# Kernel tuning notes

Hardware: AMD Instinct MI355X
Metric: run time of the kernel (lower is better)

## Reference

```python
import jax, jax.numpy as jnp
import numpy as np

T, M = 64, 64
ROI, SPA, WORD, I3D = 2048, 4, 300, 1024
H, D = 512, 256  # so_hidden, so_out_dim (= rel_dim)
IN = ROI + SPA + WORD  # 2352


def _w(k, shape):
    return jax.random.normal(k, shape, dtype=jnp.float32) * 0.02


def setup_inputs() -> dict:
    key = jax.random.key(0)
    ks = jax.random.split(key, 32)
    inp = {
        "roi_feats": jax.random.normal(ks[0], (T, M, ROI), dtype=jnp.float32),
        "spatial": jax.random.uniform(ks[1], (T, M, SPA), dtype=jnp.float32),
        "i3d_feats": jax.random.normal(ks[2], (T, I3D), dtype=jnp.float32),
        "subj_emb": jax.random.normal(ks[3], (WORD,), dtype=jnp.float32),
        "obj_emb": jax.random.normal(ks[4], (WORD,), dtype=jnp.float32),
        "pred_emb": jax.random.normal(ks[5], (WORD,), dtype=jnp.float32),
        # subject / object encoders (torch Linear convention: W is (out,in))
        "subj_w1": _w(ks[6], (H, IN)), "subj_b1": _w(ks[7], (H,)),
        "subj_w2": _w(ks[8], (D, H)), "subj_b2": _w(ks[9], (D,)),
        "obj_w1": _w(ks[10], (H, IN)), "obj_b1": _w(ks[11], (H,)),
        "obj_w2": _w(ks[12], (D, H)), "obj_b2": _w(ks[13], (D,)),
        # fuse MLPs (in = 2*D)
        "fuse_s_w1": _w(ks[14], (H, 2 * D)), "fuse_s_b1": _w(ks[15], (H,)),
        "fuse_s_w2": _w(ks[16], (D, H)), "fuse_s_b2": _w(ks[17], (D,)),
        "fuse_o_w1": _w(ks[18], (H, 2 * D)), "fuse_o_b1": _w(ks[19], (H,)),
        "fuse_o_w2": _w(ks[20], (D, H)), "fuse_o_b2": _w(ks[21], (D,)),
        # relation projections + MLP
        "W_rs": _w(ks[22], (D, D)),
        "W_ro": _w(ks[23], (D, D)),
        "rel_w1": _w(ks[24], (H, D + WORD)), "rel_b1": _w(ks[25], (H,)),
        "rel_w2": _w(ks[26], (D, H)), "rel_b2": _w(ks[27], (D,)),
    }
    return inp


def _linear(x, W, b):
    return x @ W.T + b


def _mlp2(x, w1, b1, w2, b2):
    return _linear(jax.nn.relu(_linear(x, w1, b1)), w2, b2)


def reference(roi_feats, spatial, i3d_feats, subj_emb, obj_emb, pred_emb,
              subj_w1, subj_b1, subj_w2, subj_b2,
              obj_w1, obj_b1, obj_w2, obj_b2,
              fuse_s_w1, fuse_s_b1, fuse_s_w2, fuse_s_b2,
              fuse_o_w1, fuse_o_b1, fuse_o_w2, fuse_o_b2,
              W_rs, W_ro, rel_w1, rel_b1, rel_w2, rel_b2):
    Tn, Mn, _ = roi_feats.shape
    se = jnp.broadcast_to(subj_emb, (Tn, Mn, subj_emb.shape[-1]))
    oe = jnp.broadcast_to(obj_emb, (Tn, Mn, obj_emb.shape[-1]))
    # SubjectObjectEncoder: fc2(relu(fc1([roi; spa; word])))
    fs_base = _mlp2(jnp.concatenate([roi_feats, spatial, se], axis=-1),
                    subj_w1, subj_b1, subj_w2, subj_b2)  # (T,M,D)
    fo_base = _mlp2(jnp.concatenate([roi_feats, spatial, oe], axis=-1),
                    obj_w1, obj_b1, obj_w2, obj_b2)
    # use_gsa = use_lla = False -> fuse([base; base])
    fs = _mlp2(jnp.concatenate([fs_base, fs_base], axis=-1),
               fuse_s_w1, fuse_s_b1, fuse_s_w2, fuse_s_b2)
    fo = _mlp2(jnp.concatenate([fo_base, fo_base], axis=-1),
               fuse_o_w1, fuse_o_b1, fuse_o_w2, fuse_o_b2)
    # Eq. 15: pairwise diff + predicate word, then 2-layer MLP
    fs_proj = fs @ W_rs.T
    fo_proj = fo @ W_ro.T
    diff = fs_proj[:, :, None, :] - fo_proj[:, None, :, :]  # (T,M,M,D)
    # rel_fc1([diff; pred]) split into diff part + constant pred part
    Wd, Wp = rel_w1[:, :fs.shape[-1]], rel_w1[:, fs.shape[-1]:]
    h = jax.nn.relu(diff @ Wd.T + (pred_emb @ Wp.T + rel_b1))  # (T,M,M,H)
    return h @ rel_w2.T + rel_b2  # (T,M,M,D)
```

## Files before the change

kernel.cpp:

```cpp
#include <hip/hip_runtime.h>
#include <hip/hip_bf16.h>

typedef __attribute__((ext_vector_type(4))) float f32x4;
typedef __attribute__((ext_vector_type(8))) short s16x8;

__device__ __forceinline__ void async_lds16(const void* g, void* l) {
  __builtin_amdgcn_global_load_lds((const __attribute__((address_space(1))) void*)g,
                                   (__attribute__((address_space(3))) void*)l, 16, 0, 0);
}

__device__ __forceinline__ short f2bf(float x) {
  __hip_bfloat16 h = __float2bfloat16(x);
  short s;
  __builtin_memcpy(&s, &h, 2);
  return s;
}

__device__ __forceinline__ s16x8 pack8(f32x4 a, f32x4 b) {
  s16x8 r;
  r[0] = f2bf(a[0]); r[1] = f2bf(a[1]); r[2] = f2bf(a[2]); r[3] = f2bf(a[3]);
  r[4] = f2bf(b[0]); r[5] = f2bf(b[1]); r[6] = f2bf(b[2]); r[7] = f2bf(b[3]);
  return r;
}

template<bool RELU, bool OUT_BF16, bool HAS_BIAS>
__global__ __launch_bounds__(256) void gemm_bt(
    const __hip_bfloat16* __restrict__ Ag, const __hip_bfloat16* __restrict__ Bg,
    const float* __restrict__ biasg, void* __restrict__ Cg,
    int lda, int ldb, int K, int ldc,
    int strideA, int strideB, int strideBias, long strideC)
{
  __shared__ __align__(16) short As[4096];
  __shared__ __align__(16) short Bs[4096];
  const int tid  = threadIdx.x;
  const int lane = tid & 63;
  const int wid  = tid >> 6;
  const int z    = blockIdx.z;
  const __hip_bfloat16* A = Ag + (long)z * strideA;
  const __hip_bfloat16* B = Bg + (long)z * strideB;
  const float* bias = HAS_BIAS ? (biasg + (long)z * strideBias) : nullptr;
  const int row0 = blockIdx.y * 128;
  const int col0 = blockIdx.x * 128;

  const int srow = wid * 16 + (lane >> 2);
  const int scol = (lane & 3) * 8;

  f32x4 acc[4][4];
#pragma unroll
  for (int i = 0; i < 4; ++i)
#pragma unroll
    for (int j = 0; j < 4; ++j) acc[i][j] = (f32x4)(0.0f);

  const int rw = (wid & 1) * 64;
  const int cw = (wid >> 1) * 64;
  const int lm = lane & 15;
  const int kg = (lane >> 4) * 8;

  for (int ks = 0; ks < K; ks += 32) {
    __syncthreads();
#pragma unroll
    for (int is = 0; is < 2; ++is) {
      async_lds16(A + (long)(row0 + is * 64 + srow) * lda + ks + scol,
                  (char*)As + is * 4096 + wid * 1024);
      async_lds16(B + (long)(col0 + is * 64 + srow) * ldb + ks + scol,
                  (char*)Bs + is * 4096 + wid * 1024);
    }
    __syncthreads();
    s16x8 af[4], bf[4];
#pragma unroll
    for (int mt = 0; mt < 4; ++mt)
      af[mt] = *(const s16x8*)(As + (rw + mt * 16 + lm) * 32 + kg);
#pragma unroll
    for (int nt = 0; nt < 4; ++nt)
      bf[nt] = *(const s16x8*)(Bs + (cw + nt * 16 + lm) * 32 + kg);
#pragma unroll
    for (int mt = 0; mt < 4; ++mt)
#pragma unroll
      for (int nt = 0; nt < 4; ++nt)
        acc[mt][nt] = __builtin_amdgcn_mfma_f32_16x16x32_bf16(af[mt], bf[nt], acc[mt][nt], 0, 0, 0);
  }

  const int lr4 = (lane >> 4) * 4;
#pragma unroll
  for (int mt = 0; mt < 4; ++mt) {
#pragma unroll
    for (int nt = 0; nt < 4; ++nt) {
      const int col = col0 + cw + nt * 16 + lm;
      const float bv = HAS_BIAS ? bias[col] : 0.0f;
#pragma unroll
      for (int r = 0; r < 4; ++r) {
        const int row = row0 + rw + mt * 16 + lr4 + r;
        float v = acc[mt][nt][r] + bv;
        if (RELU) v = fmaxf(v, 0.0f);
        if (OUT_BF16)
          ((__hip_bfloat16*)Cg)[(long)z * strideC + (long)row * ldc + col] = __float2bfloat16(v);
        else
          ((float*)Cg)[(long)z * strideC + (long)row * ldc + col] = v;
      }
    }
  }
}

template<bool RELU, bool OUT_BF16, bool HAS_BIAS>
__global__ __launch_bounds__(256) void gemm_bt64(
    const __hip_bfloat16* __restrict__ Ag, const __hip_bfloat16* __restrict__ Bg,
    const float* __restrict__ biasg, void* __restrict__ Cg,
    int lda, int ldb, int K, int ldc,
    int strideA, int strideB, int strideBias, long strideC)
{
  __shared__ __align__(16) short As[2048];
  __shared__ __align__(16) short Bs[2048];
  const int tid  = threadIdx.x;
  const int lane = tid & 63;
  const int wid  = tid >> 6;
  const int z    = blockIdx.z;
  const __hip_bfloat16* A = Ag + (long)z * strideA;
  const __hip_bfloat16* B = Bg + (long)z * strideB;
  const float* bias = HAS_BIAS ? (biasg + (long)z * strideBias) : nullptr;
  const int row0 = blockIdx.y * 64;
  const int col0 = blockIdx.x * 64;

  const int srow = wid * 16 + (lane >> 2);
  const int scol = (lane & 3) * 8;

  f32x4 acc[2][2];
#pragma unroll
  for (int i = 0; i < 2; ++i)
#pragma unroll
    for (int j = 0; j < 2; ++j) acc[i][j] = (f32x4)(0.0f);

  const int rw = (wid & 1) * 32;
  const int cw = (wid >> 1) * 32;
  const int lm = lane & 15;
  const int kg = (lane >> 4) * 8;

  for (int ks = 0; ks < K; ks += 32) {
    __syncthreads();
    async_lds16(A + (long)(row0 + srow) * lda + ks + scol, (char*)As + wid * 1024);
    async_lds16(B + (long)(col0 + srow) * ldb + ks + scol, (char*)Bs + wid * 1024);
    __syncthreads();
    s16x8 af[2], bf[2];
#pragma unroll
    for (int mt = 0; mt < 2; ++mt)
      af[mt] = *(const s16x8*)(As + (rw + mt * 16 + lm) * 32 + kg);
#pragma unroll
    for (int nt = 0; nt < 2; ++nt)
      bf[nt] = *(const s16x8*)(Bs + (cw + nt * 16 + lm) * 32 + kg);
#pragma unroll
    for (int mt = 0; mt < 2; ++mt)
#pragma unroll
      for (int nt = 0; nt < 2; ++nt)
        acc[mt][nt] = __builtin_amdgcn_mfma_f32_16x16x32_bf16(af[mt], bf[nt], acc[mt][nt], 0, 0, 0);
  }

  const int lr4 = (lane >> 4) * 4;
#pragma unroll
  for (int mt = 0; mt < 2; ++mt) {
#pragma unroll
    for (int nt = 0; nt < 2; ++nt) {
      const int col = col0 + cw + nt * 16 + lm;
      const float bv = HAS_BIAS ? bias[col] : 0.0f;
#pragma unroll
      for (int r = 0; r < 4; ++r) {
        const int row = row0 + rw + mt * 16 + lr4 + r;
        float v = acc[mt][nt][r] + bv;
        if (RELU) v = fmaxf(v, 0.0f);
        if (OUT_BF16)
          ((__hip_bfloat16*)Cg)[(long)z * strideC + (long)row * ldc + col] = __float2bfloat16(v);
        else
          ((float*)Cg)[(long)z * strideC + (long)row * ldc + col] = v;
      }
    }
  }
}

__global__ __launch_bounds__(256) void reduce_relu(
    const float* __restrict__ P, const float* __restrict__ cboth,
    __hip_bfloat16* __restrict__ H1)
{
  const int id = blockIdx.x * 256 + threadIdx.x;
  const int row = id >> 7, c8 = id & 127;
  const f32x4* p0 = (const f32x4*)(P + (long)row * 1024 + c8 * 8);
  const f32x4* p1 = (const f32x4*)(P + 4194304 + (long)row * 1024 + c8 * 8);
  const f32x4* bb = (const f32x4*)(cboth + c8 * 8);
  f32x4 a = p0[0] + p1[0] + bb[0];
  f32x4 b = p0[1] + p1[1] + bb[1];
#pragma unroll
  for (int e = 0; e < 4; ++e) { a[e] = fmaxf(a[e], 0.0f); b[e] = fmaxf(b[e], 0.0f); }
  *(s16x8*)((short*)H1 + (long)row * 1024 + c8 * 8) = pack8(a, b);
}

__global__ __launch_bounds__(256) void rel_final(
    const float* __restrict__ AsBo, const __hip_bfloat16* __restrict__ W2b,
    const float* __restrict__ b2, float* __restrict__ out)
{
  __shared__ __align__(16) short Hs[4096];
  __shared__ __align__(16) short Ws[4096];
  const int tid  = threadIdx.x;
  const int lane = tid & 63;
  const int wid  = tid >> 6;
  const int n0 = blockIdx.x * 128;
  const int i0 = blockIdx.y * 2;
  const int t  = blockIdx.z;

  const float* Ap = AsBo + (long)(t * 64 + i0) * 512;
  const float* Bp = AsBo + 2097152 + (long)t * 64 * 512;

  const int grow = tid >> 1;
  const int gkc  = (tid & 1) * 16;
  const float* arow = Ap + (grow >> 6) * 512 + gkc;
  const float* brow = Bp + (grow & 63) * 512 + gkc;
  short* hdst = Hs + grow * 32 + gkc;

  const int srow = wid * 16 + (lane >> 2);
  const int scol = (lane & 3) * 8;

  f32x4 acc[4][4];
#pragma unroll
  for (int i = 0; i < 4; ++i)
#pragma unroll
    for (int j = 0; j < 4; ++j) acc[i][j] = (f32x4)(0.0f);

  const int rw = (wid & 1) * 64;
  const int cw = (wid >> 1) * 64;
  const int lm = lane & 15;
  const int kg = (lane >> 4) * 8;

  for (int ks = 0; ks < 512; ks += 32) {
    __syncthreads();
#pragma unroll
    for (int is = 0; is < 2; ++is)
      async_lds16(W2b + (long)(n0 + is * 64 + srow) * 512 + ks + scol,
                  (char*)Ws + is * 4096 + wid * 1024);
    f32x4 av[4], bv[4];
#pragma unroll
    for (int q = 0; q < 4; ++q) {
      av[q] = *(const f32x4*)(arow + ks + q * 4);
      bv[q] = *(const f32x4*)(brow + ks + q * 4);
    }
    union { s16x8 v; short s[8]; } p0, p1;
#pragma unroll
    for (int q = 0; q < 2; ++q)
#pragma unroll
      for (int e = 0; e < 4; ++e) {
        p0.s[q * 4 + e] = f2bf(fmaxf(av[q][e] - bv[q][e], 0.0f));
        p1.s[q * 4 + e] = f2bf(fmaxf(av[q + 2][e] - bv[q + 2][e], 0.0f));
      }
    *(s16x8*)hdst = p0.v;
    *(s16x8*)(hdst + 8) = p1.v;
    __syncthreads();
    s16x8 af[4], bf[4];
#pragma unroll
    for (int mt = 0; mt < 4; ++mt)
      af[mt] = *(const s16x8*)(Hs + (rw + mt * 16 + lm) * 32 + kg);
#pragma unroll
    for (int nt = 0; nt < 4; ++nt)
      bf[nt] = *(const s16x8*)(Ws + (cw + nt * 16 + lm) * 32 + kg);
#pragma unroll
    for (int mt = 0; mt < 4; ++mt)
#pragma unroll
      for (int nt = 0; nt < 4; ++nt)
        acc[mt][nt] = __builtin_amdgcn_mfma_f32_16x16x32_bf16(af[mt], bf[nt], acc[mt][nt], 0, 0, 0);
  }

  const int lr4 = (lane >> 4) * 4;
#pragma unroll
  for (int mt = 0; mt < 4; ++mt) {
#pragma unroll
    for (int nt = 0; nt < 4; ++nt) {
      const int col = n0 + cw + nt * 16 + lm;
      const float bv = b2[col];
#pragma unroll
      for (int r = 0; r < 4; ++r) {
        const int prow = rw + mt * 16 + lr4 + r;
        const int il = prow >> 6, j = prow & 63;
        out[(long)((t * 64 + i0 + il) * 64 + j) * 256 + col] = acc[mt][nt][r] + bv;
      }
    }
  }
}

__global__ __launch_bounds__(256) void prep_kernel(
    const float* __restrict__ roi, const float* __restrict__ spatial,
    const float* __restrict__ subj_emb, const float* __restrict__ obj_emb,
    const float* __restrict__ pred_emb,
    const float* __restrict__ subj_w1, const float* __restrict__ subj_b1,
    const float* __restrict__ obj_w1, const float* __restrict__ obj_b1,
    const float* __restrict__ subj_w2, const float* __restrict__ subj_b2,
    const float* __restrict__ obj_w2, const float* __restrict__ obj_b2,
    const float* __restrict__ fs_w1, const float* __restrict__ fs_b1,
    const float* __restrict__ fs_w2, const float* __restrict__ fs_b2,
    const float* __restrict__ fo_w1, const float* __restrict__ fo_b1,
    const float* __restrict__ fo_w2, const float* __restrict__ fo_b2,
    const float* __restrict__ W_rs, const float* __restrict__ W_ro,
    const float* __restrict__ rel_w1, const float* __restrict__ rel_b1,
    const float* __restrict__ rel_w2,
    __hip_bfloat16* __restrict__ XP, __hip_bfloat16* __restrict__ W1P,
    float* __restrict__ cboth,
    __hip_bfloat16* __restrict__ Bcat2, float* __restrict__ bias2,
    __hip_bfloat16* __restrict__ WfCat, float* __restrict__ biasf,
    __hip_bfloat16* __restrict__ W4cat, float* __restrict__ bias4,
    __hip_bfloat16* __restrict__ WcCat, float* __restrict__ crel,
    __hip_bfloat16* __restrict__ W2b)
{
  int id = blockIdx.x * 256 + threadIdx.x;

  if (id < 1081344) {
    int row = id / 264, c8 = id - row * 264;
    s16x8 o;
    if (c8 < 256) {
      const f32x4* src = (const f32x4*)(roi + (long)row * 2048 + c8 * 8);
      o = pack8(src[0], src[1]);
    } else {
      f32x4 a, b;
#pragma unroll
      for (int e = 0; e < 4; ++e) {
        int col = c8 * 8 + e;
        a[e] = (col < 2052) ? spatial[row * 4 + (col - 2048)] : 0.0f;
        int col2 = col + 4;
        b[e] = (col2 < 2052) ? spatial[row * 4 + (col2 - 2048)] : 0.0f;
      }
      o = pack8(a, b);
    }
    *(s16x8*)((short*)XP + (long)id * 8) = o;
    return;
  }
  id -= 1081344;
  if (id < 270336) {
    int row = id / 264, c8 = id - row * 264;
    const float* w = (row < 512) ? (subj_w1 + (long)row * 2352)
                                 : (obj_w1 + (long)(row - 512) * 2352);
    s16x8 o;
    if (c8 < 256) {
      const f32x4* src = (const f32x4*)(w + c8 * 8);
      o = pack8(src[0], src[1]);
    } else {
      f32x4 a, b;
#pragma unroll
      for (int e = 0; e < 4; ++e) {
        int col = c8 * 8 + e;
        a[e] = (col < 2052) ? w[col] : 0.0f;
        int col2 = col + 4;
        b[e] = (col2 < 2052) ? w[col2] : 0.0f;
      }
      o = pack8(a, b);
    }
    *(s16x8*)((short*)W1P + (long)id * 8) = o;
    return;
  }
  id -= 270336;
  if (id < 1024) {
    int h = id;
    const float* w; const float* e; float s;
    if (h < 512) { w = subj_w1 + (long)h * 2352 + 2052; e = subj_emb; s = subj_b1[h]; }
    else { w = obj_w1 + (long)(h - 512) * 2352 + 2052; e = obj_emb; s = obj_b1[h - 512]; }
    for (int k = 0; k < 300; ++k) s += w[k] * e[k];
    cboth[h] = s;
    return;
  }
  id -= 1024;
  if (id < 32768) {
    const float* src = (id < 16384) ? (subj_w2 + id * 8) : (obj_w2 + (id - 16384) * 8);
    const f32x4* s4 = (const f32x4*)src;
    *(s16x8*)((short*)Bcat2 + (long)id * 8) = pack8(s4[0], s4[1]);
    return;
  }
  id -= 32768;
  if (id < 512) { bias2[id] = (id < 256) ? subj_b2[id] : obj_b2[id - 256]; return; }
  id -= 512;
  if (id < 32768) {
    int z = id >> 14, r8 = id & 16383;
    int h = r8 >> 5, d8 = r8 & 31;
    const float* w = (z ? fo_w1 : fs_w1) + h * 512 + d8 * 8;
    const f32x4* lo = (const f32x4*)w;
    const f32x4* hi = (const f32x4*)(w + 256);
    *(s16x8*)((short*)WfCat + (long)id * 8) = pack8(lo[0] + hi[0], lo[1] + hi[1]);
    return;
  }
  id -= 32768;
  if (id < 1024) { biasf[id] = (id < 512) ? fs_b1[id] : fo_b1[id - 512]; return; }
  id -= 1024;
  if (id < 32768) {
    const float* src = (id < 16384) ? (fs_w2 + id * 8) : (fo_w2 + (id - 16384) * 8);
    const f32x4* s4 = (const f32x4*)src;
    *(s16x8*)((short*)W4cat + (long)id * 8) = pack8(s4[0], s4[1]);
    return;
  }
  id -= 32768;
  if (id < 512) { bias4[id] = (id < 256) ? fs_b2[id] : fo_b2[id - 256]; return; }
  id -= 512;
  if (id < 262144) {
    int z = id >> 17, r = id & 131071;
    int h = r >> 8, d = r & 255;
    const float* Wr = z ? W_ro : W_rs;
    const float* wd = rel_w1 + (long)h * 556;
    float s = 0.0f;
    for (int e = 0; e < 256; ++e) s += wd[e] * Wr[e * 256 + d];
    WcCat[id] = __float2bfloat16(s);
    return;
  }
  id -= 262144;
  if (id < 1024) {
    int z = id >> 9, h = id & 511;
    float s = 0.0f;
    if (z == 0) {
      s = rel_b1[h];
      const float* wp = rel_w1 + (long)h * 556 + 256;
      for (int k = 0; k < 300; ++k) s += pred_emb[k] * wp[k];
    }
    crel[id] = s;
    return;
  }
  id -= 1024;
  if (id < 16384) {
    const f32x4* s4 = (const f32x4*)(rel_w2 + id * 8);
    *(s16x8*)((short*)W2b + (long)id * 8) = pack8(s4[0], s4[1]);
  }
}

extern "C" void kernel_launch(void* const* d_in, const int* in_sizes, int n_in,
                              void* d_out, int out_size, void* d_ws, size_t ws_size,
                              hipStream_t stream)
{
  const float* roi       = (const float*)d_in[0];
  const float* spatial   = (const float*)d_in[1];
  const float* subj_emb  = (const float*)d_in[3];
  const float* obj_emb   = (const float*)d_in[4];
  const float* pred_emb  = (const float*)d_in[5];
  const float* subj_w1   = (const float*)d_in[6];
  const float* subj_b1   = (const float*)d_in[7];
  const float* subj_w2   = (const float*)d_in[8];
  const float* subj_b2   = (const float*)d_in[9];
  const float* obj_w1    = (const float*)d_in[10];
  const float* obj_b1    = (const float*)d_in[11];
  const float* obj_w2    = (const float*)d_in[12];
  const float* obj_b2    = (const float*)d_in[13];
  const float* fuse_s_w1 = (const float*)d_in[14];
  const float* fuse_s_b1 = (const float*)d_in[15];
  const float* fuse_s_w2 = (const float*)d_in[16];
  const float* fuse_s_b2 = (const float*)d_in[17];
  const float* fuse_o_w1 = (const float*)d_in[18];
  const float* fuse_o_b1 = (const float*)d_in[19];
  const float* fuse_o_w2 = (const float*)d_in[20];
  const float* fuse_o_b2 = (const float*)d_in[21];
  const float* W_rs      = (const float*)d_in[22];
  const float* W_ro      = (const float*)d_in[23];
  const float* rel_w1    = (const float*)d_in[24];
  const float* rel_b1    = (const float*)d_in[25];
  const float* rel_w2    = (const float*)d_in[26];
  const float* rel_b2    = (const float*)d_in[27];

  char* ws = (char*)d_ws;
  __hip_bfloat16* XP   = (__hip_bfloat16*)(ws);
  float*          AsBo = (float*)(ws);
  __hip_bfloat16* W1P  = (__hip_bfloat16*)(ws + 17301504);
  __hip_bfloat16* H1   = (__hip_bfloat16*)(ws + 21626880);
  __hip_bfloat16* FS   = (__hip_bfloat16*)(ws + 30015488);
  float*          P    = (float*)(ws + 34209792);
  const size_t so = 67764224;
  __hip_bfloat16* Bcat2 = (__hip_bfloat16*)(ws + so);
  float*          bias2 = (float*)(ws + so + 524288);
  __hip_bfloat16* WfCat = (__hip_bfloat16*)(ws + so + 526336);
  float*          biasf = (float*)(ws + so + 1050624);
  __hip_bfloat16* W4cat = (__hip_bfloat16*)(ws + so + 1054720);
  float*          bias4 = (float*)(ws + so + 1579008);
  __hip_bfloat16* WcCat = (__hip_bfloat16*)(ws + so + 1581056);
  float*          crel  = (float*)(ws + so + 2105344);
  __hip_bfloat16* W2b   = (__hip_bfloat16*)(ws + so + 2109440);
  float*          cboth = (float*)(ws + so + 2371584);

  prep_kernel<<<6768, 256, 0, stream>>>(
      roi, spatial, subj_emb, obj_emb, pred_emb,
      subj_w1, subj_b1, obj_w1, obj_b1, subj_w2, subj_b2, obj_w2, obj_b2,
      fuse_s_w1, fuse_s_b1, fuse_s_w2, fuse_s_b2,
      fuse_o_w1, fuse_o_b1, fuse_o_w2, fuse_o_b2,
      W_rs, W_ro, rel_w1, rel_b1, rel_w2,
      XP, W1P, cboth, Bcat2, bias2, WfCat, biasf, W4cat, bias4, WcCat, crel, W2b);

  gemm_bt<false, false, false><<<dim3(8, 32, 2), 256, 0, stream>>>(
      XP, W1P, cboth, P, 2112, 2112, 1056, 1024, 1056, 1056, 0, 4194304L);
  reduce_relu<<<2048, 256, 0, stream>>>(P, cboth, H1);
  gemm_bt64<false, true, true><<<dim3(4, 64, 2), 256, 0, stream>>>(
      H1, Bcat2, bias2, FS, 1024, 512, 512, 512, 512, 131072, 256, 256);
  gemm_bt64<true, true, true><<<dim3(8, 64, 2), 256, 0, stream>>>(
      FS, WfCat, biasf, H1, 512, 256, 256, 1024, 256, 131072, 512, 512);
  gemm_bt64<false, true, true><<<dim3(4, 64, 2), 256, 0, stream>>>(
      H1, W4cat, bias4, FS, 1024, 512, 512, 512, 512, 131072, 256, 256);
  gemm_bt64<false, false, true><<<dim3(8, 64, 2), 256, 0, stream>>>(
      FS, WcCat, crel, AsBo, 512, 256, 256, 512, 256, 131072, 512, 2097152L);
  rel_final<<<dim3(2, 32, 64), 256, 0, stream>>>(AsBo, W2b, rel_b2, (float*)d_out);
}
```

Measured before the change: 574.5 us.

## Build relu-diff A fragments in registers and widen rel_final tile to full N

rel_final now computes the relu(As-Bo) bf16 MFMA A-fragments directly in registers from global memory instead of staging them through LDS. Each block also covers all 256 output columns (4x8 accumulator tiles per wave), so the diff computation is no longer repeated across two column blocks. This drops an LDS round trip and halves redundant diff work, at the cost of more accumulator registers (128 floats per lane), which may reduce occupancy. Each wave also loads B rows from global directly, with possible redundancy across waves.

```diff
diff --git a/kernel.cpp b/kernel.cpp
--- a/kernel.cpp
+++ b/kernel.cpp
@@ -194,87 +194,74 @@
     const float* __restrict__ AsBo, const __hip_bfloat16* __restrict__ W2b,
     const float* __restrict__ b2, float* __restrict__ out)
 {
-  __shared__ __align__(16) short Hs[4096];
-  __shared__ __align__(16) short Ws[4096];
+  __shared__ __align__(16) short Ws[8192];
   const int tid  = threadIdx.x;
   const int lane = tid & 63;
   const int wid  = tid >> 6;
-  const int n0 = blockIdx.x * 128;
-  const int i0 = blockIdx.y * 2;
-  const int t  = blockIdx.z;
-
-  const float* Ap = AsBo + (long)(t * 64 + i0) * 512;
-  const float* Bp = AsBo + 2097152 + (long)t * 64 * 512;
-
-  const int grow = tid >> 1;
-  const int gkc  = (tid & 1) * 16;
-  const float* arow = Ap + (grow >> 6) * 512 + gkc;
-  const float* brow = Bp + (grow & 63) * 512 + gkc;
-  short* hdst = Hs + grow * 32 + gkc;
-
-  const int srow = wid * 16 + (lane >> 2);
-  const int scol = (lane & 3) * 8;
-
-  f32x4 acc[4][4];
-#pragma unroll
-  for (int i = 0; i < 4; ++i)
-#pragma unroll
-    for (int j = 0; j < 4; ++j) acc[i][j] = (f32x4)(0.0f);
-
-  const int rw = (wid & 1) * 64;
-  const int cw = (wid >> 1) * 64;
+  const int i0 = blockIdx.x;
+  const int t  = blockIdx.y;
+
+  const int il = wid & 1;
+  const int cw = (wid >> 1) * 128;
   const int lm = lane & 15;
   const int kg = (lane >> 4) * 8;
 
+  const float* arow = AsBo + (long)(t * 64 + i0 * 2 + il) * 512;
+  const float* Bp   = AsBo + 2097152 + (long)t * 64 * 512;
+
+  f32x4 acc[4][8];
+#pragma unroll
+  for (int i = 0; i < 4; ++i)
+#pragma unroll
+    for (int j = 0; j < 8; ++j) acc[i][j] = (f32x4)(0.0f);
+
   for (int ks = 0; ks < 512; ks += 32) {
     __syncthreads();
 #pragma unroll
-    for (int is = 0; is < 2; ++is)
-      async_lds16(W2b + (long)(n0 + is * 64 + srow) * 512 + ks + scol,
+    for (int is = 0; is < 4; ++is) {
+      const int r = is * 64 + wid * 16 + (lane >> 2);
+      async_lds16(W2b + (long)r * 512 + ks + (lane & 3) * 8,
                   (char*)Ws + is * 4096 + wid * 1024);
-    f32x4 av[4], bv[4];
-#pragma unroll
-    for (int q = 0; q < 4; ++q) {
-      av[q] = *(const f32x4*)(arow + ks + q * 4);
-      bv[q] = *(const f32x4*)(brow + ks + q * 4);
-    }
-    union { s16x8 v; short s[8]; } p0, p1;
-#pragma unroll
-    for (int q = 0; q < 2; ++q)
+    }
+    const f32x4 av0 = *(const f32x4*)(arow + ks + kg);
+    const f32x4 av1 = *(const f32x4*)(arow + ks + kg + 4);
+    s16x8 af[4];
+#pragma unroll
+    for (int mt = 0; mt < 4; ++mt) {
+      const float* brow = Bp + (long)(mt * 16 + lm) * 512 + ks + kg;
+      f32x4 d0 = av0 - *(const f32x4*)(brow);
+      f32x4 d1 = av1 - *(const f32x4*)(brow + 4);
 #pragma unroll
       for (int e = 0; e < 4; ++e) {
-        p0.s[q * 4 + e] = f2bf(fmaxf(av[q][e] - bv[q][e], 0.0f));
-        p1.s[q * 4 + e] = f2bf(fmaxf(av[q + 2][e] - bv[q + 2][e], 0.0f));
-      }
-    *(s16x8*)hdst = p0.v;
-    *(s16x8*)(hdst + 8) = p1.v;
-    __syncthreads();
-    s16x8 af[4], bf[4];
+        d0[e] = fmaxf(d0[e], 0.0f);
+        d1[e] = fmaxf(d1[e], 0.0f);
+      }
+      af[mt] = pack8(d0, d1);
+    }
+    __syncthreads();
+    s16x8 bf[8];
+#pragma unroll
+    for (int nt = 0; nt < 8; ++nt)
+      bf[nt] = *(const s16x8*)(Ws + (cw + nt * 16 + lm) * 32 + kg);
 #pragma unroll
     for (int mt = 0; mt < 4; ++mt)
-      af[mt] = *(const s16x8*)(Hs + (rw + mt * 16 + lm) * 32 + kg);
-#pragma unroll
-    for (int nt = 0; nt < 4; ++nt)
-      bf[nt] = *(const s16x8*)(Ws + (cw + nt * 16 + lm) * 32 + kg);
-#pragma unroll
-    for (int mt = 0; mt < 4; ++mt)
-#pragma unroll
-      for (int nt = 0; nt < 4; ++nt)
+#pragma unroll
+      for (int nt = 0; nt < 8; ++nt)
         acc[mt][nt] = __builtin_amdgcn_mfma_f32_16x16x32_bf16(af[mt], bf[nt], acc[mt][nt], 0, 0, 0);
   }
 
   const int lr4 = (lane >> 4) * 4;
+  float* orow = out + (long)(t * 64 + i0 * 2 + il) * 64 * 256;
 #pragma unroll
   for (int mt = 0; mt < 4; ++mt) {
 #pragma unroll
-    for (int nt = 0; nt < 4; ++nt) {
-      const int col = n0 + cw + nt * 16 + lm;
-      const float bv = b2[col];
+    for (int nt = 0; nt < 8; ++nt) {
+      const int col = cw + nt * 16 + lm;
+      const float bb = b2[col];
 #pragma unroll
       for (int r = 0; r < 4; ++r) {
-        const int prow = rw + mt * 16 + lr4 + r;
-        const int il = prow >> 6, j = prow & 63;
-        out[(long)((t * 64 + i0 + il) * 64 + j) * 256 + col] = acc[mt][nt][r] + bv;
+        const int j = mt * 16 + lr4 + r;
+        orow[(long)j * 256 + col] = acc[mt][nt][r] + bb;
       }
     }
   }
@@ -488,5 +475,5 @@
       H1, W4cat, bias4, FS, 1024, 512, 512, 512, 512, 131072, 256, 256);
   gemm_bt64<false, false, true><<<dim3(8, 64, 2), 256, 0, stream>>>(
       FS, WcCat, crel, AsBo, 512, 256, 256, 512, 256, 131072, 512, 2097152L);
-  rel_final<<<dim3(2, 32, 64), 256, 0, stream>>>(AsBo, W2b, rel_b2, (float*)d_out);
-}
+  rel_final<<<dim3(32, 64), 256, 0, stream>>>(AsBo, W2b, rel_b2, (float*)d_out);
+}
```

Measured after the change: 680.2 us. +18.4%, slower.
